# Kernel optimization log

Hardware: AMD Instinct MI355X
Metric: run time of the kernel (lower is better)

## Reference

```python
import jax, jax.numpy as jnp
import numpy as np
import math

IMAGE_SIZE = 256
VIEWING_ANGLE = 30.0  # degrees
NEAR = 0.1
FAR = 100.0
CHUNK = 50


def _look_at(vertices):
    # nr.look_at with at=origin, up=+y, eye from viewing_angle (as in __init__)
    eye = jnp.array([0.0, 0.0, -(1.0 / math.tan(math.radians(VIEWING_ANGLE)) + 1.0)],
                    dtype=vertices.dtype)
    at = jnp.zeros(3, dtype=vertices.dtype)
    up = jnp.array([0.0, 1.0, 0.0], dtype=vertices.dtype)
    z = at - eye
    z = z / jnp.linalg.norm(z)
    x = jnp.cross(up, z)
    x = x / jnp.linalg.norm(x)
    y = jnp.cross(z, x)
    y = y / jnp.linalg.norm(y)
    R = jnp.stack([x, y, z])  # [3,3] rows = camera axes
    return (vertices - eye) @ R.T


def _perspective(v):
    # nr.perspective: x,y divided by z*tan(angle); z (camera depth) kept
    width = math.tan(math.radians(VIEWING_ANGLE))
    z = v[..., 2]
    zs = jnp.where(jnp.abs(z) < 1e-5, 1e-5, z)  # avoid div-by-zero for behind-camera verts
    return jnp.stack([v[..., 0] / (zs * width), v[..., 1] / (zs * width), z], axis=-1)


def reference(vertices, faces):
    """Renderer.forward(vertices, faces, mode='depth'):
    fill_back -> look_at -> perspective -> vertices_to_faces -> rasterize_depth.
    Returns depth image [B, H, W] (FAR where no face covers the pixel)."""
    B = vertices.shape[0]
    # fill_back: append faces with reversed vertex order
    faces2 = jnp.concatenate([faces, faces[:, :, ::-1]], axis=1)  # [B, 2F, 3]
    v_scr = _perspective(_look_at(vertices))                      # [B, V, 3]
    # vertices_to_faces gather
    fv = jax.vmap(lambda v, f: v[f])(v_scr, faces2)               # [B, 2F, 3, 3]
    F2 = fv.shape[1]
    nsteps = F2 // CHUNK
    fv = fv.reshape(B, nsteps, CHUNK, 3, 3).transpose(1, 0, 2, 3, 4)  # [S,B,C,3,3]

    is_ = IMAGE_SIZE
    p = (2.0 * jnp.arange(is_, dtype=vertices.dtype) + 1.0 - is_) / is_  # pixel centers in (-1,1)
    py, px = jnp.meshgrid(p, p, indexing='ij')  # [H,W]

    def step(buf, f):  # f: [B,C,3,3]; z-buffer min over this face chunk
        x = f[..., 0][..., None, None]  # [B,C,3,1,1]
        y = f[..., 1][..., None, None]
        z = f[..., 2]                   # [B,C,3] camera-space depth per vertex
        x0, x1, x2 = x[:, :, 0], x[:, :, 1], x[:, :, 2]
        y0, y1, y2 = y[:, :, 0], y[:, :, 1], y[:, :, 2]
        area = (x1 - x0) * (y2 - y0) - (x2 - x0) * (y1 - y0)  # [B,C,1,1] signed 2*area
        area_s = jnp.where(jnp.abs(area) < 1e-8, 1e-8, area)
        # screen-space barycentric weights (edge functions / area)
        w0 = ((x1 - px) * (y2 - py) - (x2 - px) * (y1 - py)) / area_s
        w1 = ((x2 - px) * (y0 - py) - (x0 - px) * (y2 - py)) / area_s
        w2 = 1.0 - w0 - w1
        zc = jnp.maximum(z, 1e-4)  # safe for masked-out faces only
        # perspective-correct depth: z = 1 / (w0/z0 + w1/z1 + w2/z2)
        inv_z = (w0 / zc[:, :, 0, None, None] + w1 / zc[:, :, 1, None, None]
                 + w2 / zc[:, :, 2, None, None])
        zp = 1.0 / jnp.maximum(inv_z, 1e-6)
        front = jnp.all(z > NEAR, axis=-1)[..., None, None]
        inside = (w0 >= 0) & (w1 >= 0) & (w2 >= 0) & (jnp.abs(area) > 1e-8)
        valid = inside & front & (zp > NEAR) & (zp < FAR)
        zp = jnp.where(valid, zp, FAR)
        return jnp.minimum(buf, jnp.min(zp, axis=1)), None

    buf0 = jnp.full((B, is_, is_), FAR, dtype=vertices.dtype)
    depth, _ = jax.lax.scan(step, buf0, fv)
    return depth


def setup_inputs() -> dict:
    key = jax.random.key(0)
    kv, kf = jax.random.split(key)
    B, NV, NF = 1, 2502, 5000
    # mesh roughly within the camera frustum (eye at z~-2.73 looking at origin)
    vertices = 0.35 * jax.random.normal(kv, (B, NV, 3), dtype=jnp.float32)
    faces = jax.random.randint(kf, (B, NF, 3), 0, NV, dtype=jnp.int32)
    return {"vertices": vertices, "faces": faces}
```

## Files before the change

kernel.cpp:

```cpp
#include <hip/hip_runtime.h>

#define IS 256
#define NEARV 0.1f
#define FARV 100.0f
#define NTX 16
#define NTILES 256
#define CAP 5120
#define CHK 32
#define CPT ((CAP + CHK - 1) / CHK)
#define RBLOCKS 2048
#define RWAVES (RBLOCKS * 4)
#define MAXITEMS (NTILES * CPT)

__global__ void kinit(unsigned int* __restrict__ zb, int* __restrict__ count,
                      int* __restrict__ misc) {
    int i = blockIdx.x * 256 + threadIdx.x;
    zb[i] = 0x42C80000u;
    if (i < NTILES) count[i] = 0;
    if (i == NTILES) misc[0] = 0;
}

__launch_bounds__(256)
__global__ void kbinprep(const float* __restrict__ verts, const int* __restrict__ faces,
                         float4* __restrict__ fd, int* __restrict__ count,
                         unsigned short* __restrict__ list, int* __restrict__ misc,
                         int* __restrict__ items, int nf) {
    __shared__ int scnt[NTILES];
    __shared__ int sbase[NTILES];
    __shared__ int slast;
    const int tid = threadIdx.x;
    for (int t = tid; t < NTILES; t += 256) scnt[t] = 0;
    __syncthreads();

    const int f = blockIdx.x * 256 + tid;
    int kx0 = 0, kx1 = -1, ky0 = 0, ky1 = -1;
    float bxmin = 0.f, bymin = 0.f, bxmax = -1.f, bymax = -1.f;
    if (f < nf) {
        int i0 = faces[f * 3 + 0];
        int i1 = faces[f * 3 + 1];
        int i2 = faces[f * 3 + 2];
        float z0 = verts[i0 * 3 + 2] + 2.7320508075688772f;
        float z1 = verts[i1 * 3 + 2] + 2.7320508075688772f;
        float z2 = verts[i2 * 3 + 2] + 2.7320508075688772f;
        bool front = (z0 > NEARV) && (z1 > NEARV) && (z2 > NEARV);
        float zs0 = (fabsf(z0) < 1e-5f) ? 1e-5f : z0;
        float zs1 = (fabsf(z1) < 1e-5f) ? 1e-5f : z1;
        float zs2 = (fabsf(z2) < 1e-5f) ? 1e-5f : z2;
        float d0 = zs0 * 0.57735026918962576f;
        float d1 = zs1 * 0.57735026918962576f;
        float d2 = zs2 * 0.57735026918962576f;
        float x0 = verts[i0 * 3 + 0] / d0;
        float y0 = verts[i0 * 3 + 1] / d0;
        float x1 = verts[i1 * 3 + 0] / d1;
        float y1 = verts[i1 * 3 + 1] / d1;
        float x2 = verts[i2 * 3 + 0] / d2;
        float y2 = verts[i2 * 3 + 1] / d2;
        float area = (x1 - x0) * (y2 - y0) - (x2 - x0) * (y1 - y0);
        if (front && (fabsf(area) > 1e-8f)) {
            bxmin = fminf(x0, fminf(x1, x2));
            bxmax = fmaxf(x0, fmaxf(x1, x2));
            bymin = fminf(y0, fminf(y1, y2));
            bymax = fmaxf(y0, fmaxf(y1, y2));
            float ia = 1.0f / area;
            float iz0 = 1.0f / fmaxf(z0, 1e-4f);
            float iz1 = 1.0f / fmaxf(z1, 1e-4f);
            float iz2 = 1.0f / fmaxf(z2, 1e-4f);
            float4* o = fd + (size_t)f * 4;
            o[0] = make_float4(x0, y0, x1, y1);
            o[1] = make_float4(x2, y2, ia, iz0);
            o[2] = make_float4(iz1, iz2, 0.0f, 0.0f);
            float tminx = fminf(fmaxf((bxmin * 256.0f + 225.0f) * (1.0f / 32.0f), -2.0f), 17.0f);
            float tmaxx = fminf(fmaxf((bxmax * 256.0f + 255.0f) * (1.0f / 32.0f), -2.0f), 17.0f);
            float tminy = fminf(fmaxf((bymin * 256.0f + 225.0f) * (1.0f / 32.0f), -2.0f), 17.0f);
            float tmaxy = fminf(fmaxf((bymax * 256.0f + 255.0f) * (1.0f / 32.0f), -2.0f), 17.0f);
            kx0 = max(0, (int)ceilf(tminx) - 1);
            kx1 = min(NTX - 1, (int)floorf(tmaxx) + 1);
            ky0 = max(0, (int)ceilf(tminy) - 1);
            ky1 = min(NTX - 1, (int)floorf(tmaxy) + 1);
        }
    }
    for (int ky = ky0; ky <= ky1; ++ky) {
        float py_lo = (float)(32 * ky - 255) * (1.0f / 256.0f);
        float py_hi = (float)(32 * ky - 225) * (1.0f / 256.0f);
        if (!(bymin <= py_hi && bymax >= py_lo)) continue;
        for (int kx = kx0; kx <= kx1; ++kx) {
            float px_lo = (float)(32 * kx - 255) * (1.0f / 256.0f);
            float px_hi = (float)(32 * kx - 225) * (1.0f / 256.0f);
            if (bxmin <= px_hi && bxmax >= px_lo) atomicAdd(&scnt[ky * NTX + kx], 1);
        }
    }
    __syncthreads();
    for (int t = tid; t < NTILES; t += 256) {
        int c = scnt[t];
        sbase[t] = (c > 0) ? atomicAdd(&count[t], c) : 0;
        scnt[t] = 0;
    }
    __syncthreads();
    for (int ky = ky0; ky <= ky1; ++ky) {
        float py_lo = (float)(32 * ky - 255) * (1.0f / 256.0f);
        float py_hi = (float)(32 * ky - 225) * (1.0f / 256.0f);
        if (!(bymin <= py_hi && bymax >= py_lo)) continue;
        for (int kx = kx0; kx <= kx1; ++kx) {
            float px_lo = (float)(32 * kx - 255) * (1.0f / 256.0f);
            float px_hi = (float)(32 * kx - 225) * (1.0f / 256.0f);
            if (bxmin <= px_hi && bxmax >= px_lo) {
                int t = ky * NTX + kx;
                int slot = sbase[t] + atomicAdd(&scnt[t], 1);
                list[(size_t)t * CAP + slot] = (unsigned short)f;
            }
        }
    }
    __syncthreads();
    __threadfence();
    if (tid == 0) slast = (atomicAdd(&misc[0], 1) == (int)gridDim.x - 1) ? 1 : 0;
    __syncthreads();
    if (!slast) return;
    __threadfence();
    int c = __hip_atomic_load(&count[tid], __ATOMIC_RELAXED, __HIP_MEMORY_SCOPE_AGENT);
    int nch = (c + CHK - 1) / CHK;
    scnt[tid] = nch;
    __syncthreads();
    for (int d = 1; d < NTILES; d <<= 1) {
        int v = (tid >= d) ? scnt[tid - d] : 0;
        __syncthreads();
        scnt[tid] += v;
        __syncthreads();
    }
    int off = scnt[tid] - nch;
    if (tid == NTILES - 1) misc[64] = scnt[tid];
    for (int k = 0; k < nch; ++k) {
        int n = min(CHK, c - k * CHK);
        items[off + k] = (tid << 16) | (n << 8) | k;
    }
}

__launch_bounds__(256)
__global__ void kraster(const float4* __restrict__ fd, const unsigned short* __restrict__ list,
                        const int* __restrict__ items, const int* __restrict__ misc,
                        unsigned int* __restrict__ zb) {
    __shared__ float4 sdata[4][CHK * 3];
    const int wslot = __builtin_amdgcn_readfirstlane(threadIdx.x >> 6);
    const int wid = blockIdx.x * 4 + wslot;
    const int lane = threadIdx.x & 63;
    const int cx = lane & 15;
    const int ry = lane >> 4;
    const int ni = __builtin_amdgcn_readfirstlane(misc[64]);
    float4* sd = &sdata[wslot][0];

    for (int it = wid; it < ni; it += RWAVES) {
        const int pk = __builtin_amdgcn_readfirstlane(items[it]);
        const int tile = pk >> 16;
        const int n = (pk >> 8) & 0xff;
        const int chunk = pk & 0xff;
        const int bx = tile & 15;
        const int by = tile >> 4;
        const int j = bx * 16 + cx;
        const float px = ((float)(2 * j + 1) - 256.0f) * (1.0f / 256.0f);
        float py[4];
        int row[4];
        unsigned int zcur[4];
#pragma unroll
        for (int r = 0; r < 4; ++r) {
            row[r] = by * 16 + ry + 4 * r;
            py[r] = ((float)(2 * row[r] + 1) - 256.0f) * (1.0f / 256.0f);
            zcur[r] = zb[row[r] * IS + j];
        }
        const unsigned short* lp = list + (size_t)tile * CAP + chunk * CHK;
        if (lane < n) {
            const int fidx = lp[lane];
            const float4* p = fd + (size_t)fidx * 4;
            float4 b0 = p[0];
            float4 b1 = p[1];
            float4 b2 = p[2];
            sd[lane * 3 + 0] = b0;
            sd[lane * 3 + 1] = b1;
            sd[lane * 3 + 2] = b2;
        }
        asm volatile("s_waitcnt lgkmcnt(0)" ::: "memory");

        float mx[4] = {0.0f, 0.0f, 0.0f, 0.0f};

#pragma unroll 2
        for (int e = 0; e < n; ++e) {
            float4 a0 = sd[e * 3 + 0];
            float4 a1 = sd[e * 3 + 1];
            float4 a2 = sd[e * 3 + 2];
            float dx0 = a0.x - px, dx1 = a0.z - px, dx2 = a1.x - px;
#pragma unroll
            for (int r = 0; r < 4; ++r) {
                float dy0 = a0.y - py[r], dy1 = a0.w - py[r], dy2 = a1.y - py[r];
                float e0 = dx1 * dy2 - dx2 * dy1;
                float e1 = dx2 * dy0 - dx0 * dy2;
                float w0 = e0 * a1.z;
                float w1 = e1 * a1.z;
                float w2 = 1.0f - w0 - w1;
                float invz = w0 * a1.w + w1 * a2.x + w2 * a2.y;
                float invzc = fmaxf(invz, 1e-6f);
                float wmin = fminf(fminf(w0, w1), w2);
                bool ok = (wmin >= 0.0f) && (invzc < 10.0f) && (invzc > 0.01f);
                if (ok) mx[r] = fmaxf(mx[r], invzc);
            }
        }
#pragma unroll
        for (int r = 0; r < 4; ++r) {
            if (mx[r] > 0.0f) {
                float zp = 1.0f / mx[r];
                unsigned int zbits = __float_as_uint(zp);
                if (zbits < zcur[r]) atomicMin(&zb[row[r] * IS + j], zbits);
            }
        }
    }
}

extern "C" void kernel_launch(void* const* d_in, const int* in_sizes, int n_in,
                              void* d_out, int out_size, void* d_ws, size_t ws_size,
                              hipStream_t stream) {
    const float* verts = (const float*)d_in[0];
    const int* faces = (const int*)d_in[1];
    unsigned int* zb = (unsigned int*)d_out;

    const int nf = in_sizes[1] / 3;

    char* ws = (char*)d_ws;
    size_t off = 0;
    float4* fd = (float4*)(ws + off);            off += (size_t)nf * 64;
    off = (off + 255) & ~(size_t)255;
    int* count = (int*)(ws + off);               off += NTILES * 4;
    off = (off + 255) & ~(size_t)255;
    int* misc = (int*)(ws + off);                off += 512;
    int* items = (int*)(ws + off);               off += (size_t)MAXITEMS * 4;
    off = (off + 255) & ~(size_t)255;
    unsigned short* list = (unsigned short*)(ws + off);

    const int nb = (nf + 255) / 256;

    kinit<<<(IS * IS) / 256, 256, 0, stream>>>(zb, count, misc);
    kbinprep<<<nb, 256, 0, stream>>>(verts, faces, fd, count, list, misc, items, nf);
    kraster<<<RBLOCKS, 256, 0, stream>>>(fd, list, items, misc, zb);
}
```

Measured before the change: 107.8 us.

## Replace last-block item scan with static tile/chunk wave mapping in raster

Removes the last-block-done counter, prefix scan and packed work-item list from the binning kernel. The raster kernel now maps each wave directly to a (tile, chunk-slot) pair and loops over chunks with stride 32. Each wave keeps its per-pixel max across all of its chunks and issues one atomicMin at the end, which cuts global atomics and the serial tail of binning. The cost is possible load imbalance, since tiles with many faces are handled by at most 32 waves.

Measured after the change: 156.0 us. 44.8% more time.

```diff
diff --git a/kernel.cpp b/kernel.cpp
--- a/kernel.cpp
+++ b/kernel.cpp
@@ -7,27 +7,22 @@
 #define NTILES 256
 #define CAP 5120
 #define CHK 32
-#define CPT ((CAP + CHK - 1) / CHK)
+#define CPT (CAP / CHK)
 #define RBLOCKS 2048
 #define RWAVES (RBLOCKS * 4)
-#define MAXITEMS (NTILES * CPT)
-
-__global__ void kinit(unsigned int* __restrict__ zb, int* __restrict__ count,
-                      int* __restrict__ misc) {
+
+__global__ void kinit(unsigned int* __restrict__ zb, int* __restrict__ count) {
     int i = blockIdx.x * 256 + threadIdx.x;
     zb[i] = 0x42C80000u;
     if (i < NTILES) count[i] = 0;
-    if (i == NTILES) misc[0] = 0;
 }
 
 __launch_bounds__(256)
 __global__ void kbinprep(const float* __restrict__ verts, const int* __restrict__ faces,
                          float4* __restrict__ fd, int* __restrict__ count,
-                         unsigned short* __restrict__ list, int* __restrict__ misc,
-                         int* __restrict__ items, int nf) {
+                         unsigned short* __restrict__ list, int nf) {
     __shared__ int scnt[NTILES];
     __shared__ int sbase[NTILES];
-    __shared__ int slast;
     const int tid = threadIdx.x;
     for (int t = tid; t < NTILES; t += 256) scnt[t] = 0;
     __syncthreads();
@@ -110,62 +105,44 @@
             }
         }
     }
-    __syncthreads();
-    __threadfence();
-    if (tid == 0) slast = (atomicAdd(&misc[0], 1) == (int)gridDim.x - 1) ? 1 : 0;
-    __syncthreads();
-    if (!slast) return;
-    __threadfence();
-    int c = __hip_atomic_load(&count[tid], __ATOMIC_RELAXED, __HIP_MEMORY_SCOPE_AGENT);
-    int nch = (c + CHK - 1) / CHK;
-    scnt[tid] = nch;
-    __syncthreads();
-    for (int d = 1; d < NTILES; d <<= 1) {
-        int v = (tid >= d) ? scnt[tid - d] : 0;
-        __syncthreads();
-        scnt[tid] += v;
-        __syncthreads();
-    }
-    int off = scnt[tid] - nch;
-    if (tid == NTILES - 1) misc[64] = scnt[tid];
-    for (int k = 0; k < nch; ++k) {
-        int n = min(CHK, c - k * CHK);
-        items[off + k] = (tid << 16) | (n << 8) | k;
-    }
 }
 
 __launch_bounds__(256)
 __global__ void kraster(const float4* __restrict__ fd, const unsigned short* __restrict__ list,
-                        const int* __restrict__ items, const int* __restrict__ misc,
-                        unsigned int* __restrict__ zb) {
+                        const int* __restrict__ count, unsigned int* __restrict__ zb) {
     __shared__ float4 sdata[4][CHK * 3];
     const int wslot = __builtin_amdgcn_readfirstlane(threadIdx.x >> 6);
     const int wid = blockIdx.x * 4 + wslot;
     const int lane = threadIdx.x & 63;
     const int cx = lane & 15;
     const int ry = lane >> 4;
-    const int ni = __builtin_amdgcn_readfirstlane(misc[64]);
     float4* sd = &sdata[wslot][0];
 
-    for (int it = wid; it < ni; it += RWAVES) {
-        const int pk = __builtin_amdgcn_readfirstlane(items[it]);
-        const int tile = pk >> 16;
-        const int n = (pk >> 8) & 0xff;
-        const int chunk = pk & 0xff;
-        const int bx = tile & 15;
-        const int by = tile >> 4;
-        const int j = bx * 16 + cx;
-        const float px = ((float)(2 * j + 1) - 256.0f) * (1.0f / 256.0f);
-        float py[4];
-        int row[4];
-        unsigned int zcur[4];
+    const int tile = wid & 255;
+    const int cc = wid >> 8;
+    const int c = count[tile];
+    const int nch = (c + CHK - 1) / CHK;
+    if (cc >= nch) return;
+
+    const int bx = tile & 15;
+    const int by = tile >> 4;
+    const int j = bx * 16 + cx;
+    const float px = ((float)(2 * j + 1) - 256.0f) * (1.0f / 256.0f);
+    float py[4];
+    int row[4];
+    unsigned int zcur[4];
 #pragma unroll
-        for (int r = 0; r < 4; ++r) {
-            row[r] = by * 16 + ry + 4 * r;
-            py[r] = ((float)(2 * row[r] + 1) - 256.0f) * (1.0f / 256.0f);
-            zcur[r] = zb[row[r] * IS + j];
-        }
-        const unsigned short* lp = list + (size_t)tile * CAP + chunk * CHK;
+    for (int r = 0; r < 4; ++r) {
+        row[r] = by * 16 + ry + 4 * r;
+        py[r] = ((float)(2 * row[r] + 1) - 256.0f) * (1.0f / 256.0f);
+        zcur[r] = zb[row[r] * IS + j];
+    }
+
+    float mx[4] = {0.0f, 0.0f, 0.0f, 0.0f};
+
+    for (int k = cc; k < nch; k += 32) {
+        const int n = min(CHK, c - k * CHK);
+        const unsigned short* lp = list + (size_t)tile * CAP + k * CHK;
         if (lane < n) {
             const int fidx = lp[lane];
             const float4* p = fd + (size_t)fidx * 4;
@@ -177,8 +154,6 @@
             sd[lane * 3 + 2] = b2;
         }
         asm volatile("s_waitcnt lgkmcnt(0)" ::: "memory");
-
-        float mx[4] = {0.0f, 0.0f, 0.0f, 0.0f};
 
 #pragma unroll 2
         for (int e = 0; e < n; ++e) {
@@ -201,13 +176,13 @@
                 if (ok) mx[r] = fmaxf(mx[r], invzc);
             }
         }
+    }
 #pragma unroll
-        for (int r = 0; r < 4; ++r) {
-            if (mx[r] > 0.0f) {
-                float zp = 1.0f / mx[r];
-                unsigned int zbits = __float_as_uint(zp);
-                if (zbits < zcur[r]) atomicMin(&zb[row[r] * IS + j], zbits);
-            }
+    for (int r = 0; r < 4; ++r) {
+        if (mx[r] > 0.0f) {
+            float zp = 1.0f / mx[r];
+            unsigned int zbits = __float_as_uint(zp);
+            if (zbits < zcur[r]) atomicMin(&zb[row[r] * IS + j], zbits);
         }
     }
 }
@@ -227,14 +202,11 @@
     off = (off + 255) & ~(size_t)255;
     int* count = (int*)(ws + off);               off += NTILES * 4;
     off = (off + 255) & ~(size_t)255;
-    int* misc = (int*)(ws + off);                off += 512;
-    int* items = (int*)(ws + off);               off += (size_t)MAXITEMS * 4;
-    off = (off + 255) & ~(size_t)255;
     unsigned short* list = (unsigned short*)(ws + off);
 
     const int nb = (nf + 255) / 256;
 
-    kinit<<<(IS * IS) / 256, 256, 0, stream>>>(zb, count, misc);
-    kbinprep<<<nb, 256, 0, stream>>>(verts, faces, fd, count, list, misc, items, nf);
-    kraster<<<RBLOCKS, 256, 0, stream>>>(fd, list, items, misc, zb);
-}
+    kinit<<<(IS * IS) / 256, 256, 0, stream>>>(zb, count);
+    kbinprep<<<nb, 256, 0, stream>>>(verts, faces, fd, count, list, nf);
+    kraster<<<RBLOCKS, 256, 0, stream>>>(fd, list, count, zb);
+}
```

## Fold z-buffer init into binning kernel and zero counters with memset

Applied to the files above, without the earlier changes.

Removes the separate init kernel. The z-buffer fill to FAR now happens inside the binning kernel as a grid-stride loop of vector stores, and the tile counters and misc flags are cleared with hipMemsetAsync, which requires count and misc to sit next to each other in the workspace. The binning block size grows to 1024 threads, with tile-indexed steps guarded to the first 256 threads. Fewer, larger blocks give less parallelism for the per-face work and more contention on the shared-memory atomics. The memset may also carry launch overhead comparable to the kernel it replaces.

Measured after the change: 115.3 us. 1.07x slower.

```diff
diff --git a/kernel.cpp b/kernel.cpp
--- a/kernel.cpp
+++ b/kernel.cpp
@@ -11,28 +11,30 @@
 #define RBLOCKS 2048
 #define RWAVES (RBLOCKS * 4)
 #define MAXITEMS (NTILES * CPT)
-
-__global__ void kinit(unsigned int* __restrict__ zb, int* __restrict__ count,
-                      int* __restrict__ misc) {
-    int i = blockIdx.x * 256 + threadIdx.x;
-    zb[i] = 0x42C80000u;
-    if (i < NTILES) count[i] = 0;
-    if (i == NTILES) misc[0] = 0;
-}
-
-__launch_bounds__(256)
+#define BTH 1024
+
+__launch_bounds__(BTH)
 __global__ void kbinprep(const float* __restrict__ verts, const int* __restrict__ faces,
                          float4* __restrict__ fd, int* __restrict__ count,
                          unsigned short* __restrict__ list, int* __restrict__ misc,
-                         int* __restrict__ items, int nf) {
+                         int* __restrict__ items, unsigned int* __restrict__ zb, int nf) {
     __shared__ int scnt[NTILES];
     __shared__ int sbase[NTILES];
     __shared__ int slast;
     const int tid = threadIdx.x;
-    for (int t = tid; t < NTILES; t += 256) scnt[t] = 0;
-    __syncthreads();
-
-    const int f = blockIdx.x * 256 + tid;
+    const int gid = blockIdx.x * BTH + tid;
+    const int nthr = gridDim.x * BTH;
+
+    {
+        uint4* zb4 = (uint4*)zb;
+        const uint4 farv = make_uint4(0x42C80000u, 0x42C80000u, 0x42C80000u, 0x42C80000u);
+        for (int i = gid; i < (IS * IS) / 4; i += nthr) zb4[i] = farv;
+    }
+
+    if (tid < NTILES) scnt[tid] = 0;
+    __syncthreads();
+
+    const int f = gid;
     int kx0 = 0, kx1 = -1, ky0 = 0, ky1 = -1;
     float bxmin = 0.f, bymin = 0.f, bxmax = -1.f, bymax = -1.f;
     if (f < nf) {
@@ -90,10 +92,10 @@
         }
     }
     __syncthreads();
-    for (int t = tid; t < NTILES; t += 256) {
-        int c = scnt[t];
-        sbase[t] = (c > 0) ? atomicAdd(&count[t], c) : 0;
-        scnt[t] = 0;
+    if (tid < NTILES) {
+        int c = scnt[tid];
+        sbase[tid] = (c > 0) ? atomicAdd(&count[tid], c) : 0;
+        scnt[tid] = 0;
     }
     __syncthreads();
     for (int ky = ky0; ky <= ky1; ++ky) {
@@ -116,21 +118,26 @@
     __syncthreads();
     if (!slast) return;
     __threadfence();
-    int c = __hip_atomic_load(&count[tid], __ATOMIC_RELAXED, __HIP_MEMORY_SCOPE_AGENT);
-    int nch = (c + CHK - 1) / CHK;
-    scnt[tid] = nch;
+    int c = 0, nch = 0;
+    if (tid < NTILES) {
+        c = __hip_atomic_load(&count[tid], __ATOMIC_RELAXED, __HIP_MEMORY_SCOPE_AGENT);
+        nch = (c + CHK - 1) / CHK;
+        scnt[tid] = nch;
+    }
     __syncthreads();
     for (int d = 1; d < NTILES; d <<= 1) {
-        int v = (tid >= d) ? scnt[tid - d] : 0;
+        int v = (tid >= d && tid < NTILES) ? scnt[tid - d] : 0;
         __syncthreads();
-        scnt[tid] += v;
+        if (tid < NTILES) scnt[tid] += v;
         __syncthreads();
     }
-    int off = scnt[tid] - nch;
-    if (tid == NTILES - 1) misc[64] = scnt[tid];
-    for (int k = 0; k < nch; ++k) {
-        int n = min(CHK, c - k * CHK);
-        items[off + k] = (tid << 16) | (n << 8) | k;
+    if (tid < NTILES) {
+        int off = scnt[tid] - nch;
+        if (tid == NTILES - 1) misc[64] = scnt[tid];
+        for (int k = 0; k < nch; ++k) {
+            int n = min(CHK, c - k * CHK);
+            items[off + k] = (tid << 16) | (n << 8) | k;
+        }
     }
 }
 
@@ -226,15 +233,14 @@
     float4* fd = (float4*)(ws + off);            off += (size_t)nf * 64;
     off = (off + 255) & ~(size_t)255;
     int* count = (int*)(ws + off);               off += NTILES * 4;
-    off = (off + 255) & ~(size_t)255;
     int* misc = (int*)(ws + off);                off += 512;
     int* items = (int*)(ws + off);               off += (size_t)MAXITEMS * 4;
     off = (off + 255) & ~(size_t)255;
     unsigned short* list = (unsigned short*)(ws + off);
 
-    const int nb = (nf + 255) / 256;
-
-    kinit<<<(IS * IS) / 256, 256, 0, stream>>>(zb, count, misc);
-    kbinprep<<<nb, 256, 0, stream>>>(verts, faces, fd, count, list, misc, items, nf);
+    const int nb = (nf + BTH - 1) / BTH;
+
+    hipMemsetAsync(count, 0, NTILES * 4 + 512, stream);
+    kbinprep<<<nb, BTH, 0, stream>>>(verts, faces, fd, count, list, misc, items, zb, nf);
     kraster<<<RBLOCKS, 256, 0, stream>>>(fd, list, items, misc, zb);
 }
```

## Fuse init, binning and raster into one persistent kernel with flag wait

Applied to the files above, without the earlier changes.

Merges the three kernels into a single launch. The first blocks clear the z-buffer and bin faces, and the last binning block publishes the item count through a release flag. Every block spins on that flag before rasterizing. The counters are now cleared with a memset, and the raster grid drops from 2048 to 1024 blocks. The aim is to remove the gaps between kernel launches, but it relies on all blocks being co-resident, otherwise the spin-wait deadlocks, and the z-buffer clear is not explicitly ordered before raster writes from other blocks.

Result: slower. 261.6 us (+142.8%).

```diff
diff --git a/kernel.cpp b/kernel.cpp
--- a/kernel.cpp
+++ b/kernel.cpp
@@ -8,146 +8,156 @@
 #define CAP 5120
 #define CHK 32
 #define CPT ((CAP + CHK - 1) / CHK)
-#define RBLOCKS 2048
-#define RWAVES (RBLOCKS * 4)
 #define MAXITEMS (NTILES * CPT)
-
-__global__ void kinit(unsigned int* __restrict__ zb, int* __restrict__ count,
-                      int* __restrict__ misc) {
-    int i = blockIdx.x * 256 + threadIdx.x;
-    zb[i] = 0x42C80000u;
-    if (i < NTILES) count[i] = 0;
-    if (i == NTILES) misc[0] = 0;
-}
-
-__launch_bounds__(256)
-__global__ void kbinprep(const float* __restrict__ verts, const int* __restrict__ faces,
-                         float4* __restrict__ fd, int* __restrict__ count,
-                         unsigned short* __restrict__ list, int* __restrict__ misc,
-                         int* __restrict__ items, int nf) {
+#define GBLK 1024
+#define GWAVES (GBLK * 4)
+
+__launch_bounds__(256, 4)
+__global__ void kall(const float* __restrict__ verts, const int* __restrict__ faces,
+                     float4* __restrict__ fd, int* __restrict__ count,
+                     unsigned short* __restrict__ list, int* __restrict__ misc,
+                     int* __restrict__ items, unsigned int* __restrict__ zb, int nf) {
     __shared__ int scnt[NTILES];
     __shared__ int sbase[NTILES];
     __shared__ int slast;
+    __shared__ float4 sdata[4][CHK * 3];
     const int tid = threadIdx.x;
-    for (int t = tid; t < NTILES; t += 256) scnt[t] = 0;
-    __syncthreads();
-
-    const int f = blockIdx.x * 256 + tid;
-    int kx0 = 0, kx1 = -1, ky0 = 0, ky1 = -1;
-    float bxmin = 0.f, bymin = 0.f, bxmax = -1.f, bymax = -1.f;
-    if (f < nf) {
-        int i0 = faces[f * 3 + 0];
-        int i1 = faces[f * 3 + 1];
-        int i2 = faces[f * 3 + 2];
-        float z0 = verts[i0 * 3 + 2] + 2.7320508075688772f;
-        float z1 = verts[i1 * 3 + 2] + 2.7320508075688772f;
-        float z2 = verts[i2 * 3 + 2] + 2.7320508075688772f;
-        bool front = (z0 > NEARV) && (z1 > NEARV) && (z2 > NEARV);
-        float zs0 = (fabsf(z0) < 1e-5f) ? 1e-5f : z0;
-        float zs1 = (fabsf(z1) < 1e-5f) ? 1e-5f : z1;
-        float zs2 = (fabsf(z2) < 1e-5f) ? 1e-5f : z2;
-        float d0 = zs0 * 0.57735026918962576f;
-        float d1 = zs1 * 0.57735026918962576f;
-        float d2 = zs2 * 0.57735026918962576f;
-        float x0 = verts[i0 * 3 + 0] / d0;
-        float y0 = verts[i0 * 3 + 1] / d0;
-        float x1 = verts[i1 * 3 + 0] / d1;
-        float y1 = verts[i1 * 3 + 1] / d1;
-        float x2 = verts[i2 * 3 + 0] / d2;
-        float y2 = verts[i2 * 3 + 1] / d2;
-        float area = (x1 - x0) * (y2 - y0) - (x2 - x0) * (y1 - y0);
-        if (front && (fabsf(area) > 1e-8f)) {
-            bxmin = fminf(x0, fminf(x1, x2));
-            bxmax = fmaxf(x0, fmaxf(x1, x2));
-            bymin = fminf(y0, fminf(y1, y2));
-            bymax = fmaxf(y0, fmaxf(y1, y2));
-            float ia = 1.0f / area;
-            float iz0 = 1.0f / fmaxf(z0, 1e-4f);
-            float iz1 = 1.0f / fmaxf(z1, 1e-4f);
-            float iz2 = 1.0f / fmaxf(z2, 1e-4f);
-            float4* o = fd + (size_t)f * 4;
-            o[0] = make_float4(x0, y0, x1, y1);
-            o[1] = make_float4(x2, y2, ia, iz0);
-            o[2] = make_float4(iz1, iz2, 0.0f, 0.0f);
-            float tminx = fminf(fmaxf((bxmin * 256.0f + 225.0f) * (1.0f / 32.0f), -2.0f), 17.0f);
-            float tmaxx = fminf(fmaxf((bxmax * 256.0f + 255.0f) * (1.0f / 32.0f), -2.0f), 17.0f);
-            float tminy = fminf(fmaxf((bymin * 256.0f + 225.0f) * (1.0f / 32.0f), -2.0f), 17.0f);
-            float tmaxy = fminf(fmaxf((bymax * 256.0f + 255.0f) * (1.0f / 32.0f), -2.0f), 17.0f);
-            kx0 = max(0, (int)ceilf(tminx) - 1);
-            kx1 = min(NTX - 1, (int)floorf(tmaxx) + 1);
-            ky0 = max(0, (int)ceilf(tminy) - 1);
-            ky1 = min(NTX - 1, (int)floorf(tmaxy) + 1);
+    const int bid = blockIdx.x;
+    const int npb = (nf + 255) / 256;
+
+    if (bid < npb) {
+        {
+            uint4* zb4 = (uint4*)zb;
+            const uint4 farv = make_uint4(0x42C80000u, 0x42C80000u, 0x42C80000u, 0x42C80000u);
+            for (int i = bid * 256 + tid; i < (IS * IS) / 4; i += npb * 256) zb4[i] = farv;
+        }
+        for (int t = tid; t < NTILES; t += 256) scnt[t] = 0;
+        __syncthreads();
+
+        const int f = bid * 256 + tid;
+        int kx0 = 0, kx1 = -1, ky0 = 0, ky1 = -1;
+        float bxmin = 0.f, bymin = 0.f, bxmax = -1.f, bymax = -1.f;
+        if (f < nf) {
+            int i0 = faces[f * 3 + 0];
+            int i1 = faces[f * 3 + 1];
+            int i2 = faces[f * 3 + 2];
+            float z0 = verts[i0 * 3 + 2] + 2.7320508075688772f;
+            float z1 = verts[i1 * 3 + 2] + 2.7320508075688772f;
+            float z2 = verts[i2 * 3 + 2] + 2.7320508075688772f;
+            bool front = (z0 > NEARV) && (z1 > NEARV) && (z2 > NEARV);
+            float zs0 = (fabsf(z0) < 1e-5f) ? 1e-5f : z0;
+            float zs1 = (fabsf(z1) < 1e-5f) ? 1e-5f : z1;
+            float zs2 = (fabsf(z2) < 1e-5f) ? 1e-5f : z2;
+            float d0 = zs0 * 0.57735026918962576f;
+            float d1 = zs1 * 0.57735026918962576f;
+            float d2 = zs2 * 0.57735026918962576f;
+            float x0 = verts[i0 * 3 + 0] / d0;
+            float y0 = verts[i0 * 3 + 1] / d0;
+            float x1 = verts[i1 * 3 + 0] / d1;
+            float y1 = verts[i1 * 3 + 1] / d1;
+            float x2 = verts[i2 * 3 + 0] / d2;
+            float y2 = verts[i2 * 3 + 1] / d2;
+            float area = (x1 - x0) * (y2 - y0) - (x2 - x0) * (y1 - y0);
+            if (front && (fabsf(area) > 1e-8f)) {
+                bxmin = fminf(x0, fminf(x1, x2));
+                bxmax = fmaxf(x0, fmaxf(x1, x2));
+                bymin = fminf(y0, fminf(y1, y2));
+                bymax = fmaxf(y0, fmaxf(y1, y2));
+                float ia = 1.0f / area;
+                float iz0 = 1.0f / fmaxf(z0, 1e-4f);
+                float iz1 = 1.0f / fmaxf(z1, 1e-4f);
+                float iz2 = 1.0f / fmaxf(z2, 1e-4f);
+                float4* o = fd + (size_t)f * 4;
+                o[0] = make_float4(x0, y0, x1, y1);
+                o[1] = make_float4(x2, y2, ia, iz0);
+                o[2] = make_float4(iz1, iz2, 0.0f, 0.0f);
+                float tminx = fminf(fmaxf((bxmin * 256.0f + 225.0f) * (1.0f / 32.0f), -2.0f), 17.0f);
+                float tmaxx = fminf(fmaxf((bxmax * 256.0f + 255.0f) * (1.0f / 32.0f), -2.0f), 17.0f);
+                float tminy = fminf(fmaxf((bymin * 256.0f + 225.0f) * (1.0f / 32.0f), -2.0f), 17.0f);
+                float tmaxy = fminf(fmaxf((bymax * 256.0f + 255.0f) * (1.0f / 32.0f), -2.0f), 17.0f);
+                kx0 = max(0, (int)ceilf(tminx) - 1);
+                kx1 = min(NTX - 1, (int)floorf(tmaxx) + 1);
+                ky0 = max(0, (int)ceilf(tminy) - 1);
+                ky1 = min(NTX - 1, (int)floorf(tmaxy) + 1);
+            }
+        }
+        for (int ky = ky0; ky <= ky1; ++ky) {
+            float py_lo = (float)(32 * ky - 255) * (1.0f / 256.0f);
+            float py_hi = (float)(32 * ky - 225) * (1.0f / 256.0f);
+            if (!(bymin <= py_hi && bymax >= py_lo)) continue;
+            for (int kx = kx0; kx <= kx1; ++kx) {
+                float px_lo = (float)(32 * kx - 255) * (1.0f / 256.0f);
+                float px_hi = (float)(32 * kx - 225) * (1.0f / 256.0f);
+                if (bxmin <= px_hi && bxmax >= px_lo) atomicAdd(&scnt[ky * NTX + kx], 1);
+            }
+        }
+        __syncthreads();
+        for (int t = tid; t < NTILES; t += 256) {
+            int c = scnt[t];
+            sbase[t] = (c > 0) ? atomicAdd(&count[t], c) : 0;
+            scnt[t] = 0;
+        }
+        __syncthreads();
+        for (int ky = ky0; ky <= ky1; ++ky) {
+            float py_lo = (float)(32 * ky - 255) * (1.0f / 256.0f);
+            float py_hi = (float)(32 * ky - 225) * (1.0f / 256.0f);
+            if (!(bymin <= py_hi && bymax >= py_lo)) continue;
+            for (int kx = kx0; kx <= kx1; ++kx) {
+                float px_lo = (float)(32 * kx - 255) * (1.0f / 256.0f);
+                float px_hi = (float)(32 * kx - 225) * (1.0f / 256.0f);
+                if (bxmin <= px_hi && bxmax >= px_lo) {
+                    int t = ky * NTX + kx;
+                    int slot = sbase[t] + atomicAdd(&scnt[t], 1);
+                    list[(size_t)t * CAP + slot] = (unsigned short)f;
+                }
+            }
+        }
+        __threadfence();
+        __syncthreads();
+        if (tid == 0) slast = (atomicAdd(&misc[0], 1) == npb - 1) ? 1 : 0;
+        __syncthreads();
+        if (slast) {
+            __threadfence();
+            int c = __hip_atomic_load(&count[tid], __ATOMIC_RELAXED, __HIP_MEMORY_SCOPE_AGENT);
+            int nch = (c + CHK - 1) / CHK;
+            scnt[tid] = nch;
+            __syncthreads();
+            for (int d = 1; d < NTILES; d <<= 1) {
+                int v = (tid >= d) ? scnt[tid - d] : 0;
+                __syncthreads();
+                scnt[tid] += v;
+                __syncthreads();
+            }
+            int off = scnt[tid] - nch;
+            for (int k = 0; k < nch; ++k) {
+                int n = min(CHK, c - k * CHK);
+                items[off + k] = (tid << 16) | (n << 8) | k;
+            }
+            __threadfence();
+            __syncthreads();
+            if (tid == NTILES - 1)
+                __hip_atomic_store(&misc[16], scnt[tid] + 1,
+                                   __ATOMIC_RELEASE, __HIP_MEMORY_SCOPE_AGENT);
         }
     }
-    for (int ky = ky0; ky <= ky1; ++ky) {
-        float py_lo = (float)(32 * ky - 255) * (1.0f / 256.0f);
-        float py_hi = (float)(32 * ky - 225) * (1.0f / 256.0f);
-        if (!(bymin <= py_hi && bymax >= py_lo)) continue;
-        for (int kx = kx0; kx <= kx1; ++kx) {
-            float px_lo = (float)(32 * kx - 255) * (1.0f / 256.0f);
-            float px_hi = (float)(32 * kx - 225) * (1.0f / 256.0f);
-            if (bxmin <= px_hi && bxmax >= px_lo) atomicAdd(&scnt[ky * NTX + kx], 1);
+
+    if (tid == 0) {
+        while (__hip_atomic_load(&misc[16], __ATOMIC_ACQUIRE, __HIP_MEMORY_SCOPE_AGENT) == 0) {
+            __builtin_amdgcn_s_sleep(32);
+            __builtin_amdgcn_s_sleep(32);
         }
     }
     __syncthreads();
-    for (int t = tid; t < NTILES; t += 256) {
-        int c = scnt[t];
-        sbase[t] = (c > 0) ? atomicAdd(&count[t], c) : 0;
-        scnt[t] = 0;
-    }
-    __syncthreads();
-    for (int ky = ky0; ky <= ky1; ++ky) {
-        float py_lo = (float)(32 * ky - 255) * (1.0f / 256.0f);
-        float py_hi = (float)(32 * ky - 225) * (1.0f / 256.0f);
-        if (!(bymin <= py_hi && bymax >= py_lo)) continue;
-        for (int kx = kx0; kx <= kx1; ++kx) {
-            float px_lo = (float)(32 * kx - 255) * (1.0f / 256.0f);
-            float px_hi = (float)(32 * kx - 225) * (1.0f / 256.0f);
-            if (bxmin <= px_hi && bxmax >= px_lo) {
-                int t = ky * NTX + kx;
-                int slot = sbase[t] + atomicAdd(&scnt[t], 1);
-                list[(size_t)t * CAP + slot] = (unsigned short)f;
-            }
-        }
-    }
-    __syncthreads();
-    __threadfence();
-    if (tid == 0) slast = (atomicAdd(&misc[0], 1) == (int)gridDim.x - 1) ? 1 : 0;
-    __syncthreads();
-    if (!slast) return;
-    __threadfence();
-    int c = __hip_atomic_load(&count[tid], __ATOMIC_RELAXED, __HIP_MEMORY_SCOPE_AGENT);
-    int nch = (c + CHK - 1) / CHK;
-    scnt[tid] = nch;
-    __syncthreads();
-    for (int d = 1; d < NTILES; d <<= 1) {
-        int v = (tid >= d) ? scnt[tid - d] : 0;
-        __syncthreads();
-        scnt[tid] += v;
-        __syncthreads();
-    }
-    int off = scnt[tid] - nch;
-    if (tid == NTILES - 1) misc[64] = scnt[tid];
-    for (int k = 0; k < nch; ++k) {
-        int n = min(CHK, c - k * CHK);
-        items[off + k] = (tid << 16) | (n << 8) | k;
-    }
-}
-
-__launch_bounds__(256)
-__global__ void kraster(const float4* __restrict__ fd, const unsigned short* __restrict__ list,
-                        const int* __restrict__ items, const int* __restrict__ misc,
-                        unsigned int* __restrict__ zb) {
-    __shared__ float4 sdata[4][CHK * 3];
-    const int wslot = __builtin_amdgcn_readfirstlane(threadIdx.x >> 6);
-    const int wid = blockIdx.x * 4 + wslot;
-    const int lane = threadIdx.x & 63;
+    const int ni = __hip_atomic_load(&misc[16], __ATOMIC_ACQUIRE, __HIP_MEMORY_SCOPE_AGENT) - 1;
+
+    const int wslot = __builtin_amdgcn_readfirstlane(tid >> 6);
+    const int wid = bid * 4 + wslot;
+    const int lane = tid & 63;
     const int cx = lane & 15;
     const int ry = lane >> 4;
-    const int ni = __builtin_amdgcn_readfirstlane(misc[64]);
     float4* sd = &sdata[wslot][0];
 
-    for (int it = wid; it < ni; it += RWAVES) {
+    for (int it = wid; it < ni; it += GWAVES) {
         const int pk = __builtin_amdgcn_readfirstlane(items[it]);
         const int tile = pk >> 16;
         const int n = (pk >> 8) & 0xff;
@@ -226,15 +236,11 @@
     float4* fd = (float4*)(ws + off);            off += (size_t)nf * 64;
     off = (off + 255) & ~(size_t)255;
     int* count = (int*)(ws + off);               off += NTILES * 4;
-    off = (off + 255) & ~(size_t)255;
     int* misc = (int*)(ws + off);                off += 512;
     int* items = (int*)(ws + off);               off += (size_t)MAXITEMS * 4;
     off = (off + 255) & ~(size_t)255;
     unsigned short* list = (unsigned short*)(ws + off);
 
-    const int nb = (nf + 255) / 256;
-
-    kinit<<<(IS * IS) / 256, 256, 0, stream>>>(zb, count, misc);
-    kbinprep<<<nb, 256, 0, stream>>>(verts, faces, fd, count, list, misc, items, nf);
-    kraster<<<RBLOCKS, 256, 0, stream>>>(fd, list, items, misc, zb);
+    hipMemsetAsync(count, 0, NTILES * 4 + 512, stream);
+    kall<<<GBLK, 256, 0, stream>>>(verts, faces, fd, count, list, misc, items, zb, nf);
 }
```
